# Performance work log

Measured on AMD Instinct MI355X. Metric: run time of the kernel, lower is better.

Reference implementation:

```python
import jax, jax.numpy as jnp
import numpy as np

B, N, D = 2, 8192, 1024
H, DH = 16, 64
SEG = 512          # total_segment_len (num_longterm_mem_tokens = 0)
P = 16             # num_persist_mem_tokens
EPS = 1.1920929e-07  # torch RMSNorm eps=None -> finfo(float32).eps


def _rope(x, pos, theta=10000.0):
    # rotary-embedding-torch style: interleaved pairs, freqs repeated (n r), r=2
    d = x.shape[-1]
    inv_freq = 1.0 / (theta ** (jnp.arange(0, d, 2, dtype=jnp.float32) / d))  # [d/2]
    ang = pos[:, None] * inv_freq                                             # [n, d/2]
    cos = jnp.repeat(jnp.cos(ang), 2, axis=-1)                                # [n, d]
    sin = jnp.repeat(jnp.sin(ang), 2, axis=-1)
    x1, x2 = x[..., 0::2], x[..., 1::2]
    rot = jnp.stack((-x2, x1), axis=-1).reshape(x.shape)
    return x * cos + rot * sin


def setup_inputs() -> dict:
    key = jax.random.key(0)
    ks = jax.random.split(key, 5)
    return {
        "seq": jax.random.normal(ks[0], (B, N, D), dtype=jnp.float32),
        "w_norm": 1.0 + 0.02 * jax.random.normal(ks[1], (D,), dtype=jnp.float32),
        "Wqkv": jax.random.normal(ks[2], (D, 3 * H * DH), dtype=jnp.float32) * (D ** -0.5),
        "Wout": jax.random.normal(ks[3], (H * DH, D), dtype=jnp.float32) * ((H * DH) ** -0.5),
        "pm": 0.02 * jax.random.normal(ks[4], (2, H, P, DH), dtype=jnp.float32),
    }


def reference(seq, w_norm, Wqkv, Wout, pm):
    b, n, d = seq.shape
    w = n // SEG  # n is a multiple of SEG by construction

    # RMSNorm
    x = seq * jax.lax.rsqrt(jnp.mean(seq * seq, axis=-1, keepdims=True) + EPS) * w_norm

    # QKV projection, split heads -> [b, h, n, dh]
    qkv = x @ Wqkv
    q, k, v = jnp.split(qkv, 3, axis=-1)
    split = lambda t: t.reshape(b, n, H, DH).transpose(0, 2, 1, 3)
    q, k, v = split(q), split(k), split(v)

    # RoPE on full (global) positions before segmenting
    pos = jnp.arange(n, dtype=jnp.float32)
    q = _rope(q, pos)
    k = _rope(k, pos)

    # Segment: [b, h, n, dh] -> [b*w, h, SEG, dh]
    seg = lambda t: t.reshape(b, H, w, SEG, DH).transpose(0, 2, 1, 3, 4).reshape(b * w, H, SEG, DH)
    q, k, v = seg(q), seg(k), seg(v)

    # Prepend persistent memory KVs
    pmk = jnp.broadcast_to(pm[0], (b * w, H, P, DH))
    pmv = jnp.broadcast_to(pm[1], (b * w, H, P, DH))
    k = jnp.concatenate((pmk, k), axis=-2)  # [b*w, h, P+SEG, dh]
    v = jnp.concatenate((pmv, v), axis=-2)

    # Causal attention with kv offset P (persistent tokens always visible)
    scale = DH ** -0.5
    scores = jnp.einsum('bhid,bhjd->bhij', q, k) * scale  # [b*w, h, SEG, P+SEG]
    mask = (jnp.arange(P + SEG) - P)[None, :] <= jnp.arange(SEG)[:, None]
    scores = jnp.where(mask, scores, jnp.finfo(scores.dtype).min)
    attn = jax.nn.softmax(scores, axis=-1)
    out = jnp.einsum('bhij,bhjd->bhid', attn, v)  # [b*w, h, SEG, dh]

    # Merge heads, un-segment, output projection
    out = out.transpose(0, 2, 1, 3).reshape(b * w, SEG, H * DH)
    out = out @ Wout
    out = out.reshape(b, n, -1)
    return out
```

## Files before the change

### kernel.cpp

```cpp
#include <hip/hip_runtime.h>
#include <hip/hip_bf16.h>
#include <stdint.h>
#include <stddef.h>

typedef _Float16 f16;
typedef __attribute__((ext_vector_type(8))) _Float16 f16x8;
typedef __attribute__((ext_vector_type(4))) _Float16 f16x4;
typedef __attribute__((ext_vector_type(4))) float f32x4;
typedef __attribute__((ext_vector_type(16))) float f32x16;

#define MFMA_F16(a, b, c) __builtin_amdgcn_mfma_f32_16x16x32_f16(a, b, c, 0, 0, 0)
#define MFMA32_F16(a, b, c) __builtin_amdgcn_mfma_f32_32x32x16_f16(a, b, c, 0, 0, 0)

__device__ __forceinline__ uint32_t swz(uint32_t ci) {
    return (ci & ~7u) | ((ci ^ (ci >> 3)) & 7u);
}

__device__ __forceinline__ void async_ld16(void* lds, const void* g) {
    __builtin_amdgcn_global_load_lds(
        (const __attribute__((address_space(1))) void*)g,
        (__attribute__((address_space(3))) void*)lds, 16, 0, 0);
}

__global__ __launch_bounds__(256) void k_transpose_cast(
        const float* __restrict__ S, f16* __restrict__ D, int rows, int cols) {
    __shared__ float tile[32][33];
    int x = threadIdx.x & 31, y = threadIdx.x >> 5;
    int c0 = blockIdx.x * 32, r0 = blockIdx.y * 32;
#pragma unroll
    for (int i = 0; i < 32; i += 8)
        tile[y + i][x] = S[(size_t)(r0 + y + i) * cols + c0 + x];
    __syncthreads();
#pragma unroll
    for (int i = 0; i < 32; i += 8)
        D[(size_t)(c0 + y + i) * rows + r0 + x] = (f16)tile[x][y + i];
}

__global__ __launch_bounds__(256) void k_rmsnorm(
        const float* __restrict__ seq, const float* __restrict__ w, f16* __restrict__ X) {
    int row = blockIdx.x, t = threadIdx.x;
    const float4* sp = (const float4*)(seq + (size_t)row * 1024);
    float4 v = sp[t];
    float ss = v.x * v.x + v.y * v.y + v.z * v.z + v.w * v.w;
#pragma unroll
    for (int off = 32; off >= 1; off >>= 1) ss += __shfl_xor(ss, off, 64);
    __shared__ float red[4];
    if ((t & 63) == 0) red[t >> 6] = ss;
    __syncthreads();
    float tot = red[0] + red[1] + red[2] + red[3];
    float rs = rsqrtf(tot * (1.0f / 1024.0f) + 1.1920929e-07f);
    const float4* wp = (const float4*)w;
    float4 wv = wp[t];
    f16x4 o;
    o[0] = (f16)(v.x * rs * wv.x);
    o[1] = (f16)(v.y * rs * wv.y);
    o[2] = (f16)(v.z * rs * wv.z);
    o[3] = (f16)(v.w * rs * wv.w);
    *(f16x4*)(X + (size_t)row * 1024 + t * 4) = o;
}

template <bool OUTF32>
__global__ __launch_bounds__(256) void k_gemm(
        const f16* __restrict__ A, const f16* __restrict__ BT,
        void* __restrict__ Cv, int M, int N, int K) {
    __shared__ f16 As[128 * 32];
    __shared__ f16 Bs[128 * 32];
    const int t = threadIdx.x;
    const int lane = t & 63, wave = t >> 6, l32 = lane & 31, half = lane >> 5;
    const int m0 = blockIdx.y * 128, n0 = blockIdx.x * 128;
    const int wm = (wave & 1) * 64, wn = (wave >> 1) * 64;
    f32x16 acc[2][2];
#pragma unroll
    for (int i = 0; i < 2; i++)
#pragma unroll
        for (int j = 0; j < 2; j++)
#pragma unroll
            for (int r = 0; r < 16; r++) acc[i][j][r] = 0.f;

    uint32_t aoff[2][2], boff[2][2];
#pragma unroll
    for (int bk = 0; bk < 2; bk++)
#pragma unroll
        for (int ks = 0; ks < 2; ks++) {
            aoff[bk][ks] = swz((uint32_t)(wm + bk * 32 + l32) * 4 + ks * 2 + half) * 16;
            boff[bk][ks] = swz((uint32_t)(wn + bk * 32 + l32) * 4 + ks * 2 + half) * 16;
        }
    uint32_t c0 = swz(t), c1 = swz(t + 256);
    const f16* Ag0 = A + (size_t)(m0 + (c0 >> 2)) * K + (c0 & 3) * 8;
    const f16* Ag1 = A + (size_t)(m0 + (c1 >> 2)) * K + (c1 & 3) * 8;
    const f16* Bg0 = BT + (size_t)(n0 + (c0 >> 2)) * K + (c0 & 3) * 8;
    const f16* Bg1 = BT + (size_t)(n0 + (c1 >> 2)) * K + (c1 & 3) * 8;
    char* AsB = (char*)As;
    char* BsB = (char*)Bs;

    for (int k0 = 0; k0 < K; k0 += 32) {
        __syncthreads();
        async_ld16(AsB + t * 16, Ag0 + k0);
        async_ld16(AsB + (t + 256) * 16, Ag1 + k0);
        async_ld16(BsB + t * 16, Bg0 + k0);
        async_ld16(BsB + (t + 256) * 16, Bg1 + k0);
        __builtin_amdgcn_s_waitcnt(0x0f70);
        __syncthreads();
        f16x8 a[2][2], b[2][2];
#pragma unroll
        for (int bk = 0; bk < 2; bk++)
#pragma unroll
            for (int ks = 0; ks < 2; ks++) {
                a[bk][ks] = *(const f16x8*)(AsB + aoff[bk][ks]);
                b[bk][ks] = *(const f16x8*)(BsB + boff[bk][ks]);
            }
#pragma unroll
        for (int mb = 0; mb < 2; mb++)
#pragma unroll
            for (int nb = 0; nb < 2; nb++) {
                acc[mb][nb] = MFMA32_F16(b[nb][0], a[mb][0], acc[mb][nb]);
                acc[mb][nb] = MFMA32_F16(b[nb][1], a[mb][1], acc[mb][nb]);
            }
    }
#pragma unroll
    for (int mb = 0; mb < 2; mb++) {
        int row = m0 + wm + mb * 32 + l32;
#pragma unroll
        for (int nb = 0; nb < 2; nb++) {
            int colb = n0 + wn + nb * 32 + half * 4;
#pragma unroll
            for (int q = 0; q < 4; q++) {
                int col = colb + q * 8;
                if (OUTF32) {
                    f32x4 ov;
#pragma unroll
                    for (int r = 0; r < 4; r++) ov[r] = acc[mb][nb][q * 4 + r];
                    *(f32x4*)((float*)Cv + (size_t)row * N + col) = ov;
                } else {
                    f16x4 ov;
#pragma unroll
                    for (int r = 0; r < 4; r++) ov[r] = (f16)acc[mb][nb][q * 4 + r];
                    *(f16x4*)((f16*)Cv + (size_t)row * N + col) = ov;
                }
            }
        }
    }
}

__global__ __launch_bounds__(256) void k_prep(
        const f16* __restrict__ qkv, const float* __restrict__ pm,
        f16* __restrict__ Q, f16* __restrict__ Kb, f16* __restrict__ Vt) {
    const int jt = blockIdx.x, wh = blockIdx.y;
    const int bw = wh >> 4, h = wh & 15;
    const int t = threadIdx.x;
    const int g = t & 15;

#pragma unroll
    for (int it = 0; it < 4; it++) {
        int i = jt * 64 + it * 16 + (t >> 4);
        int tok = bw * 512 + i;
        int n = tok & 8191;
        const f16* qp = qkv + (size_t)tok * 3072 + h * 64 + g * 4;
        f16x4 qv = *(const f16x4*)(qp);
        f16x4 kv = *(const f16x4*)(qp + 1024);
        float q0 = qv[0], q1 = qv[1], q2 = qv[2], q3 = qv[3];
        float k0 = kv[0], k1 = kv[1], k2 = kv[2], k3 = kv[3];
        float fn = (float)n;
        float a0 = fn * exp2f(-0.41524101186092025f * (float)(2 * g));
        float a1 = fn * exp2f(-0.41524101186092025f * (float)(2 * g + 1));
        float s0, c0, s1, c1;
        sincosf(a0, &s0, &c0);
        sincosf(a1, &s1, &c1);
        f16x4 qo, ko;
        qo[0] = (f16)(q0 * c0 - q1 * s0);
        qo[1] = (f16)(q1 * c0 + q0 * s0);
        qo[2] = (f16)(q2 * c1 - q3 * s1);
        qo[3] = (f16)(q3 * c1 + q2 * s1);
        ko[0] = (f16)(k0 * c0 - k1 * s0);
        ko[1] = (f16)(k1 * c0 + k0 * s0);
        ko[2] = (f16)(k2 * c1 - k3 * s1);
        ko[3] = (f16)(k3 * c1 + k2 * s1);
        *(f16x4*)(Q + ((size_t)wh * 512 + i) * 64 + g * 4) = qo;
        *(f16x4*)(Kb + ((size_t)wh * 576 + 16 + i) * 64 + g * 4) = ko;
    }

    __shared__ f16 tile[64][72];
    {
        int jr = t >> 2, cq = (t & 3) * 16;
        const f16* src = qkv + ((size_t)(bw * 512 + jt * 64 + jr)) * 3072 + 2048 + h * 64 + cq;
        *(f16x8*)(&tile[jr][cq]) = *(const f16x8*)(src);
        *(f16x8*)(&tile[jr][cq + 8]) = *(const f16x8*)(src + 8);
        __syncthreads();
        int d = t >> 2, jq = (t & 3) * 16;
        f16* dst = Vt + ((size_t)wh * 64 + d) * 576 + 16 + jt * 64 + jq;
        f16x8 o0, o1;
#pragma unroll
        for (int jj = 0; jj < 8; jj++) o0[jj] = tile[jq + jj][d];
#pragma unroll
        for (int jj = 0; jj < 8; jj++) o1[jj] = tile[jq + 8 + jj][d];
        *(f16x8*)(dst) = o0;
        *(f16x8*)(dst + 8) = o1;
    }

    if (jt == 0) {
        const float* pk = pm + (size_t)h * 1024;
        f16* kb = Kb + (size_t)wh * 36864;
        int e0 = t * 4;
#pragma unroll
        for (int k = 0; k < 4; k++) kb[e0 + k] = (f16)pk[e0 + k];
        const float* pv = pm + 16384 + (size_t)h * 1024;
        f16* vb = Vt + (size_t)wh * 36864;
        int d = t & 63, s4 = (t >> 6) * 4;
#pragma unroll
        for (int k = 0; k < 4; k++)
            vb[(size_t)d * 576 + s4 + k] = (f16)pv[(s4 + k) * 64 + d];
    } else if (jt == 1) {
        f16* kb = Kb + (size_t)wh * 36864;
#pragma unroll
        for (int k = 0; k < 12; k++) kb[33792 + t + k * 256] = (f16)0.f;
        f16* vb = Vt + (size_t)wh * 36864;
        int d = t >> 2, rep = t & 3;
#pragma unroll
        for (int m = 0; m < 12; m++)
            vb[(size_t)d * 576 + 528 + rep * 12 + m] = (f16)0.f;
    }
}

__global__ __launch_bounds__(256) void k_attn(
        const f16* __restrict__ Q, const f16* __restrict__ Kb,
        const f16* __restrict__ Vt, f16* __restrict__ AO) {
    const int qt = blockIdx.x, wh = blockIdx.y;
    const int i0 = qt * 64;
    const int t = threadIdx.x, lane = t & 63, wave = t >> 6, quad = lane >> 4, l16 = lane & 15;
    __shared__ f16 Ks[64 * 64];
    __shared__ f16 Vs[64 * 64];
    __shared__ f16 Ps[4][16][80];

    const int ig = i0 + wave * 16 + l16;
    const f16* qptr = Q + ((size_t)wh * 512 + ig) * 64 + quad * 8;
    f16x8 qf0 = *(const f16x8*)(qptr);
    f16x8 qf1 = *(const f16x8*)(qptr + 32);

    const f32x4 zero = {0.f, 0.f, 0.f, 0.f};
    f32x4 o[4];
#pragma unroll
    for (int i = 0; i < 4; i++) o[i] = zero;
    float m_l = -1e30f, l_l = 0.f;

    uint32_t c0 = swz(t), c1 = swz(t + 256);
    const f16* kg0 = Kb + ((size_t)wh * 576 + (c0 >> 3)) * 64 + (c0 & 7) * 8;
    const f16* kg1 = Kb + ((size_t)wh * 576 + (c1 >> 3)) * 64 + (c1 & 7) * 8;
    const f16* vg0 = Vt + ((size_t)wh * 64 + (c0 >> 3)) * 576 + (c0 & 7) * 8;
    const f16* vg1 = Vt + ((size_t)wh * 64 + (c1 >> 3)) * 576 + (c1 & 7) * 8;
    char* KsB = (char*)Ks;
    char* VsB = (char*)Vs;

    uint32_t boff[4][2];
#pragma unroll
    for (int i = 0; i < 4; i++)
#pragma unroll
        for (int f = 0; f < 2; f++)
            boff[i][f] = swz((uint32_t)(i * 16 + l16) * 8 + f * 4 + quad) * 16;

    f16* psrow = &Ps[wave][l16][0];
    const int njt = (qt + 2 < 9) ? (qt + 2) : 9;

    for (int jt = 0; jt < njt; jt++) {
        const int j0 = jt * 64;
        __syncthreads();
        async_ld16(KsB + t * 16, kg0 + (size_t)j0 * 64);
        async_ld16(KsB + (t + 256) * 16, kg1 + (size_t)j0 * 64);
        async_ld16(VsB + t * 16, vg0 + j0);
        async_ld16(VsB + (t + 256) * 16, vg1 + j0);
        __builtin_amdgcn_s_waitcnt(0x0f70);
        __syncthreads();

        f32x4 s[4];
#pragma unroll
        for (int jb = 0; jb < 4; jb++) {
            f16x8 kv0 = *(const f16x8*)(KsB + boff[jb][0]);
            f16x8 kv1 = *(const f16x8*)(KsB + boff[jb][1]);
            f32x4 z = zero;
            z = MFMA_F16(kv0, qf0, z);
            z = MFMA_F16(kv1, qf1, z);
            s[jb] = z;
        }
        float mx = -1e30f;
#pragma unroll
        for (int jb = 0; jb < 4; jb++)
#pragma unroll
            for (int r = 0; r < 4; r++) {
                int jg = j0 + jb * 16 + quad * 4 + r;
                bool ok = (jg <= ig + 16) && (jg < 528);
                float val = ok ? s[jb][r] * 0.125f : -1e30f;
                s[jb][r] = val;
                mx = fmaxf(mx, val);
            }
        mx = fmaxf(mx, __shfl_xor(mx, 16, 64));
        mx = fmaxf(mx, __shfl_xor(mx, 32, 64));
        float mnew = fmaxf(m_l, mx);
        float alpha = __expf(m_l - mnew);
        m_l = mnew;
        float rsum = 0.f;
#pragma unroll
        for (int jb = 0; jb < 4; jb++) {
            f16x4 pw;
#pragma unroll
            for (int r = 0; r < 4; r++) {
                float p = __expf(s[jb][r] - mnew);
                rsum += p;
                pw[r] = (f16)p;
            }
            *(f16x4*)(psrow + jb * 16 + quad * 4) = pw;
        }
        rsum += __shfl_xor(rsum, 16, 64);
        rsum += __shfl_xor(rsum, 32, 64);
        l_l = l_l * alpha + rsum;
#pragma unroll
        for (int nd = 0; nd < 4; nd++) o[nd] *= alpha;
        __syncthreads();

        f16x8 pb0 = *(const f16x8*)(psrow + quad * 8);
        f16x8 pb1 = *(const f16x8*)(psrow + 32 + quad * 8);
#pragma unroll
        for (int nd = 0; nd < 4; nd++) {
            f16x8 v0 = *(const f16x8*)(VsB + boff[nd][0]);
            f16x8 v1 = *(const f16x8*)(VsB + boff[nd][1]);
            o[nd] = MFMA_F16(v0, pb0, o[nd]);
            o[nd] = MFMA_F16(v1, pb1, o[nd]);
        }
    }

    const int bw = wh >> 4, h = wh & 15;
    float inv = 1.f / l_l;
    f16* dst = AO + ((size_t)bw * 512 + ig) * 1024 + h * 64 + quad * 4;
#pragma unroll
    for (int nd = 0; nd < 4; nd++) {
        f16x4 ov;
#pragma unroll
        for (int r = 0; r < 4; r++) ov[r] = (f16)(o[nd][r] * inv);
        *(f16x4*)(dst + nd * 16) = ov;
    }
}

extern "C" void kernel_launch(void* const* d_in, const int* in_sizes, int n_in,
                              void* d_out, int out_size, void* d_ws, size_t ws_size,
                              hipStream_t stream) {
    const float* seq   = (const float*)d_in[0];
    const float* wnorm = (const float*)d_in[1];
    const float* Wqkv  = (const float*)d_in[2];
    const float* Wout  = (const float*)d_in[3];
    const float* pm    = (const float*)d_in[4];
    float* out = (float*)d_out;
    char* ws = (char*)d_ws;

    f16* WqkvT = (f16*)(ws + 0);
    f16* WoutT = (f16*)(ws + 6291456);
    f16* X     = (f16*)(ws + 8388608);
    f16* Qb    = X;
    f16* qkv   = (f16*)(ws + 41943040);
    f16* AO    = qkv;
    f16* Kb    = (f16*)(ws + 142606336);
    f16* Vt    = (f16*)(ws + 180355072);

    k_transpose_cast<<<dim3(96, 32), 256, 0, stream>>>(Wqkv, WqkvT, 1024, 3072);
    k_transpose_cast<<<dim3(32, 32), 256, 0, stream>>>(Wout, WoutT, 1024, 1024);
    k_rmsnorm<<<16384, 256, 0, stream>>>(seq, wnorm, X);
    k_gemm<false><<<dim3(24, 128), 256, 0, stream>>>(X, WqkvT, qkv, 16384, 3072, 1024);
    k_prep<<<dim3(8, 512), 256, 0, stream>>>(qkv, pm, Qb, Kb, Vt);
    k_attn<<<dim3(8, 512), 256, 0, stream>>>(Qb, Kb, Vt, AO);
    k_gemm<true><<<dim3(8, 128), 256, 0, stream>>>(AO, WoutT, out, 16384, 1024, 1024);
}
```

Before: 477.1 us.

## Fuse RoPE, head split and V transpose into QKV GEMM epilogue

The QKV GEMM epilogue now applies RoPE to Q and K and writes them straight into the segmented per-head buffers. It also scatters V transposed into the Vt layout, so the intermediate qkv tensor and the separate prep kernel go away. Persistent-memory and padding writes move to a small standalone kernel. This removes a full write and read of the 100MB qkv buffer, but adds sincos work in the GEMM epilogue and uncoalesced 2-byte scattered stores for V.

```diff
diff --git a/kernel.cpp b/kernel.cpp
--- a/kernel.cpp
+++ b/kernel.cpp
@@ -11,6 +11,8 @@
 
 #define MFMA_F16(a, b, c) __builtin_amdgcn_mfma_f32_16x16x32_f16(a, b, c, 0, 0, 0)
 #define MFMA32_F16(a, b, c) __builtin_amdgcn_mfma_f32_32x32x16_f16(a, b, c, 0, 0, 0)
+
+#define LOG2_10K_32 0.41524101186092025f
 
 __device__ __forceinline__ uint32_t swz(uint32_t ci) {
     return (ci & ~7u) | ((ci ^ (ci >> 3)) & 7u);
@@ -59,10 +61,10 @@
     *(f16x4*)(X + (size_t)row * 1024 + t * 4) = o;
 }
 
-template <bool OUTF32>
-__global__ __launch_bounds__(256) void k_gemm(
+__global__ __launch_bounds__(256) void k_gemm_qkv(
         const f16* __restrict__ A, const f16* __restrict__ BT,
-        void* __restrict__ Cv, int M, int N, int K) {
+        f16* __restrict__ Qb, f16* __restrict__ Kb, f16* __restrict__ Vt) {
+    const int K = 1024;
     __shared__ f16 As[128 * 32];
     __shared__ f16 Bs[128 * 32];
     const int t = threadIdx.x;
@@ -117,103 +119,150 @@
                 acc[mb][nb] = MFMA32_F16(b[nb][1], a[mb][1], acc[mb][nb]);
             }
     }
+
+    const int region = n0 >> 10;
 #pragma unroll
     for (int mb = 0; mb < 2; mb++) {
         int row = m0 + wm + mb * 32 + l32;
+        int b_ = row >> 13, n_ = row & 8191;
+        int win = n_ >> 9, i_ = n_ & 511;
+        float fn = (float)n_;
 #pragma unroll
         for (int nb = 0; nb < 2; nb++) {
             int colb = n0 + wn + nb * 32 + half * 4;
+            int cr = colb & 1023;
+            int h = cr >> 6;
+            int d0 = cr & 63;
+            int wh = ((b_ * 16 + win) << 4) + h;
+            if (region < 2) {
+                f16* base = (region == 0)
+                    ? (Qb + ((size_t)wh * 512 + i_) * 64)
+                    : (Kb + ((size_t)wh * 576 + 16 + i_) * 64);
+#pragma unroll
+                for (int q = 0; q < 4; q++) {
+                    int d = d0 + q * 8;
+                    float j0f = (float)(d >> 1);
+                    float ang0 = fn * exp2f(-LOG2_10K_32 * j0f);
+                    float ang1 = fn * exp2f(-LOG2_10K_32 * (j0f + 1.0f));
+                    float s0, c0f, s1, c1f;
+                    sincosf(ang0, &s0, &c0f);
+                    sincosf(ang1, &s1, &c1f);
+                    float x0 = (float)(f16)acc[mb][nb][q * 4 + 0];
+                    float x1 = (float)(f16)acc[mb][nb][q * 4 + 1];
+                    float x2 = (float)(f16)acc[mb][nb][q * 4 + 2];
+                    float x3 = (float)(f16)acc[mb][nb][q * 4 + 3];
+                    f16x4 ov;
+                    ov[0] = (f16)(x0 * c0f - x1 * s0);
+                    ov[1] = (f16)(x1 * c0f + x0 * s0);
+                    ov[2] = (f16)(x2 * c1f - x3 * s1);
+                    ov[3] = (f16)(x3 * c1f + x2 * s1);
+                    *(f16x4*)(base + d) = ov;
+                }
+            } else {
+                f16* vbase = Vt + (size_t)wh * 36864 + 16 + i_;
+#pragma unroll
+                for (int q = 0; q < 4; q++)
+#pragma unroll
+                    for (int r = 0; r < 4; r++)
+                        vbase[(size_t)(d0 + q * 8 + r) * 576] = (f16)acc[mb][nb][q * 4 + r];
+            }
+        }
+    }
+}
+
+__global__ __launch_bounds__(256) void k_gemm_out(
+        const f16* __restrict__ A, const f16* __restrict__ BT,
+        float* __restrict__ C, int M, int N, int K) {
+    __shared__ f16 As[128 * 32];
+    __shared__ f16 Bs[128 * 32];
+    const int t = threadIdx.x;
+    const int lane = t & 63, wave = t >> 6, l32 = lane & 31, half = lane >> 5;
+    const int m0 = blockIdx.y * 128, n0 = blockIdx.x * 128;
+    const int wm = (wave & 1) * 64, wn = (wave >> 1) * 64;
+    f32x16 acc[2][2];
+#pragma unroll
+    for (int i = 0; i < 2; i++)
+#pragma unroll
+        for (int j = 0; j < 2; j++)
+#pragma unroll
+            for (int r = 0; r < 16; r++) acc[i][j][r] = 0.f;
+
+    uint32_t aoff[2][2], boff[2][2];
+#pragma unroll
+    for (int bk = 0; bk < 2; bk++)
+#pragma unroll
+        for (int ks = 0; ks < 2; ks++) {
+            aoff[bk][ks] = swz((uint32_t)(wm + bk * 32 + l32) * 4 + ks * 2 + half) * 16;
+            boff[bk][ks] = swz((uint32_t)(wn + bk * 32 + l32) * 4 + ks * 2 + half) * 16;
+        }
+    uint32_t c0 = swz(t), c1 = swz(t + 256);
+    const f16* Ag0 = A + (size_t)(m0 + (c0 >> 2)) * K + (c0 & 3) * 8;
+    const f16* Ag1 = A + (size_t)(m0 + (c1 >> 2)) * K + (c1 & 3) * 8;
+    const f16* Bg0 = BT + (size_t)(n0 + (c0 >> 2)) * K + (c0 & 3) * 8;
+    const f16* Bg1 = BT + (size_t)(n0 + (c1 >> 2)) * K + (c1 & 3) * 8;
+    char* AsB = (char*)As;
+    char* BsB = (char*)Bs;
+
+    for (int k0 = 0; k0 < K; k0 += 32) {
+        __syncthreads();
+        async_ld16(AsB + t * 16, Ag0 + k0);
+        async_ld16(AsB + (t + 256) * 16, Ag1 + k0);
+        async_ld16(BsB + t * 16, Bg0 + k0);
+        async_ld16(BsB + (t + 256) * 16, Bg1 + k0);
+        __builtin_amdgcn_s_waitcnt(0x0f70);
+        __syncthreads();
+        f16x8 a[2][2], b[2][2];
+#pragma unroll
+        for (int bk = 0; bk < 2; bk++)
+#pragma unroll
+            for (int ks = 0; ks < 2; ks++) {
+                a[bk][ks] = *(const f16x8*)(AsB + aoff[bk][ks]);
+                b[bk][ks] = *(const f16x8*)(BsB + boff[bk][ks]);
+            }
+#pragma unroll
+        for (int mb = 0; mb < 2; mb++)
+#pragma unroll
+            for (int nb = 0; nb < 2; nb++) {
+                acc[mb][nb] = MFMA32_F16(b[nb][0], a[mb][0], acc[mb][nb]);
+                acc[mb][nb] = MFMA32_F16(b[nb][1], a[mb][1], acc[mb][nb]);
+            }
+    }
+#pragma unroll
+    for (int mb = 0; mb < 2; mb++) {
+        int row = m0 + wm + mb * 32 + l32;
+#pragma unroll
+        for (int nb = 0; nb < 2; nb++) {
+            int colb = n0 + wn + nb * 32 + half * 4;
 #pragma unroll
             for (int q = 0; q < 4; q++) {
-                int col = colb + q * 8;
-                if (OUTF32) {
-                    f32x4 ov;
-#pragma unroll
-                    for (int r = 0; r < 4; r++) ov[r] = acc[mb][nb][q * 4 + r];
-                    *(f32x4*)((float*)Cv + (size_t)row * N + col) = ov;
-                } else {
-                    f16x4 ov;
-#pragma unroll
-                    for (int r = 0; r < 4; r++) ov[r] = (f16)acc[mb][nb][q * 4 + r];
-                    *(f16x4*)((f16*)Cv + (size_t)row * N + col) = ov;
-                }
-            }
-        }
-    }
-}
-
-__global__ __launch_bounds__(256) void k_prep(
-        const f16* __restrict__ qkv, const float* __restrict__ pm,
-        f16* __restrict__ Q, f16* __restrict__ Kb, f16* __restrict__ Vt) {
-    const int jt = blockIdx.x, wh = blockIdx.y;
-    const int bw = wh >> 4, h = wh & 15;
-    const int t = threadIdx.x;
-    const int g = t & 15;
-
-#pragma unroll
-    for (int it = 0; it < 4; it++) {
-        int i = jt * 64 + it * 16 + (t >> 4);
-        int tok = bw * 512 + i;
-        int n = tok & 8191;
-        const f16* qp = qkv + (size_t)tok * 3072 + h * 64 + g * 4;
-        f16x4 qv = *(const f16x4*)(qp);
-        f16x4 kv = *(const f16x4*)(qp + 1024);
-        float q0 = qv[0], q1 = qv[1], q2 = qv[2], q3 = qv[3];
-        float k0 = kv[0], k1 = kv[1], k2 = kv[2], k3 = kv[3];
-        float fn = (float)n;
-        float a0 = fn * exp2f(-0.41524101186092025f * (float)(2 * g));
-        float a1 = fn * exp2f(-0.41524101186092025f * (float)(2 * g + 1));
-        float s0, c0, s1, c1;
-        sincosf(a0, &s0, &c0);
-        sincosf(a1, &s1, &c1);
-        f16x4 qo, ko;
-        qo[0] = (f16)(q0 * c0 - q1 * s0);
-        qo[1] = (f16)(q1 * c0 + q0 * s0);
-        qo[2] = (f16)(q2 * c1 - q3 * s1);
-        qo[3] = (f16)(q3 * c1 + q2 * s1);
-        ko[0] = (f16)(k0 * c0 - k1 * s0);
-        ko[1] = (f16)(k1 * c0 + k0 * s0);
-        ko[2] = (f16)(k2 * c1 - k3 * s1);
-        ko[3] = (f16)(k3 * c1 + k2 * s1);
-        *(f16x4*)(Q + ((size_t)wh * 512 + i) * 64 + g * 4) = qo;
-        *(f16x4*)(Kb + ((size_t)wh * 576 + 16 + i) * 64 + g * 4) = ko;
-    }
-
-    __shared__ f16 tile[64][72];
+                f32x4 ov;
+#pragma unroll
+                for (int r = 0; r < 4; r++) ov[r] = acc[mb][nb][q * 4 + r];
+                *(f32x4*)(C + (size_t)row * N + colb + q * 8) = ov;
+            }
+        }
+    }
+}
+
+__global__ __launch_bounds__(256) void k_pmpad(
+        const float* __restrict__ pm, f16* __restrict__ Kb, f16* __restrict__ Vt) {
+    int wh = blockIdx.x, h = wh & 15, t = threadIdx.x;
+    const float* pk = pm + (size_t)h * 1024;
+    f16* kb = Kb + (size_t)wh * 36864;
+    int e0 = t * 4;
+#pragma unroll
+    for (int k = 0; k < 4; k++) kb[e0 + k] = (f16)pk[e0 + k];
+#pragma unroll
+    for (int k = 0; k < 12; k++) kb[33792 + t + k * 256] = (f16)0.f;
+    const float* pv = pm + 16384 + (size_t)h * 1024;
+    f16* vb = Vt + (size_t)wh * 36864;
     {
-        int jr = t >> 2, cq = (t & 3) * 16;
-        const f16* src = qkv + ((size_t)(bw * 512 + jt * 64 + jr)) * 3072 + 2048 + h * 64 + cq;
-        *(f16x8*)(&tile[jr][cq]) = *(const f16x8*)(src);
-        *(f16x8*)(&tile[jr][cq + 8]) = *(const f16x8*)(src + 8);
-        __syncthreads();
-        int d = t >> 2, jq = (t & 3) * 16;
-        f16* dst = Vt + ((size_t)wh * 64 + d) * 576 + 16 + jt * 64 + jq;
-        f16x8 o0, o1;
-#pragma unroll
-        for (int jj = 0; jj < 8; jj++) o0[jj] = tile[jq + jj][d];
-#pragma unroll
-        for (int jj = 0; jj < 8; jj++) o1[jj] = tile[jq + 8 + jj][d];
-        *(f16x8*)(dst) = o0;
-        *(f16x8*)(dst + 8) = o1;
-    }
-
-    if (jt == 0) {
-        const float* pk = pm + (size_t)h * 1024;
-        f16* kb = Kb + (size_t)wh * 36864;
-        int e0 = t * 4;
-#pragma unroll
-        for (int k = 0; k < 4; k++) kb[e0 + k] = (f16)pk[e0 + k];
-        const float* pv = pm + 16384 + (size_t)h * 1024;
-        f16* vb = Vt + (size_t)wh * 36864;
         int d = t & 63, s4 = (t >> 6) * 4;
 #pragma unroll
         for (int k = 0; k < 4; k++)
             vb[(size_t)d * 576 + s4 + k] = (f16)pv[(s4 + k) * 64 + d];
-    } else if (jt == 1) {
-        f16* kb = Kb + (size_t)wh * 36864;
-#pragma unroll
-        for (int k = 0; k < 12; k++) kb[33792 + t + k * 256] = (f16)0.f;
-        f16* vb = Vt + (size_t)wh * 36864;
+    }
+    {
         int d = t >> 2, rep = t & 3;
 #pragma unroll
         for (int m = 0; m < 12; m++)
@@ -352,17 +401,16 @@
     f16* WqkvT = (f16*)(ws + 0);
     f16* WoutT = (f16*)(ws + 6291456);
     f16* X     = (f16*)(ws + 8388608);
-    f16* Qb    = X;
-    f16* qkv   = (f16*)(ws + 41943040);
-    f16* AO    = qkv;
-    f16* Kb    = (f16*)(ws + 142606336);
-    f16* Vt    = (f16*)(ws + 180355072);
+    f16* Qb    = (f16*)(ws + 41943040);
+    f16* AO    = (f16*)(ws + 75497472);
+    f16* Kb    = (f16*)(ws + 109051904);
+    f16* Vt    = (f16*)(ws + 146800640);
 
     k_transpose_cast<<<dim3(96, 32), 256, 0, stream>>>(Wqkv, WqkvT, 1024, 3072);
     k_transpose_cast<<<dim3(32, 32), 256, 0, stream>>>(Wout, WoutT, 1024, 1024);
     k_rmsnorm<<<16384, 256, 0, stream>>>(seq, wnorm, X);
-    k_gemm<false><<<dim3(24, 128), 256, 0, stream>>>(X, WqkvT, qkv, 16384, 3072, 1024);
-    k_prep<<<dim3(8, 512), 256, 0, stream>>>(qkv, pm, Qb, Kb, Vt);
+    k_pmpad<<<512, 256, 0, stream>>>(pm, Kb, Vt);
+    k_gemm_qkv<<<dim3(24, 128), 256, 0, stream>>>(X, WqkvT, Qb, Kb, Vt);
     k_attn<<<dim3(8, 512), 256, 0, stream>>>(Qb, Kb, Vt, AO);
-    k_gemm<true><<<dim3(8, 128), 256, 0, stream>>>(AO, WoutT, out, 16384, 1024, 1024);
-}
+    k_gemm_out<<<dim3(8, 128), 256, 0, stream>>>(AO, WoutT, out, 16384, 1024, 1024);
+}
```

After: 434.3 us. 9.0% less time.
